# Kernel tuning notes

Hardware: AMD Instinct MI355X
Metric: run time of the kernel (lower is better)

Reference implementation:

```python
import jax, jax.numpy as jnp
import numpy as np

C = 3  # RGB channels

# Scharr kernels, depthwise: shape [C_out, C_in/groups, kh, kw] = [C, 1, 3, 3]
_KX = np.array([[-3., 0., 3.], [-10., 0., 10.], [-3., 0., 3.]], dtype=np.float32)
_KY = np.array([[-3., -10., -3.], [0., 0., 0.], [3., 10., 3.]], dtype=np.float32)
KERNEL_X = jnp.tile(jnp.asarray(_KX)[None, None], (C, 1, 1, 1))
KERNEL_Y = jnp.tile(jnp.asarray(_KY)[None, None], (C, 1, 1, 1))


def _depthwise3x3(img, kernel):
    # img: [B, C, H, W]; kernel: [C, 1, 3, 3]; groups=C, stride 1, padding 1
    return jax.lax.conv_general_dilated(
        img, kernel,
        window_strides=(1, 1),
        padding=((1, 1), (1, 1)),
        dimension_numbers=('NCHW', 'OIHW', 'NCHW'),
        feature_group_count=C)


def _scharr_grad(img):
    gx = _depthwise3x3(img, KERNEL_X)
    gy = _depthwise3x3(img, KERNEL_Y)
    return jnp.abs(gx) + jnp.abs(gy)


def setup_inputs() -> dict:
    key = jax.random.key(0)
    kx, kg = jax.random.split(key)
    x = jax.random.uniform(kx, (16, 3, 512, 512), dtype=jnp.float32)
    gt = jax.random.uniform(kg, (16, 3, 512, 512), dtype=jnp.float32)
    return {"x": x, "gt": gt}


def reference(x, gt):
    loss = jnp.abs(_scharr_grad(x) - _scharr_grad(gt))
    return jnp.mean(loss)  # size_average=True
```

## Files before the change

### kernel.cpp

```cpp
#include <hip/hip_runtime.h>

#define Wd 512
#define Hd 512
#define NIMG 48
#define RB 8
#define LR (RB + 2)
#define NBLK (NIMG * (Hd / RB))
constexpr float INV_N = 1.0f / (float)((long long)NIMG * Hd * Wd);

__device__ __forceinline__ void gload_lds16(const float* g, float* l) {
    __builtin_amdgcn_global_load_lds(
        (const __attribute__((address_space(1))) void*)g,
        (__attribute__((address_space(3))) void*)l, 16, 0, 0);
}

__device__ __forceinline__ float scharr_pix(const float r0[10], const float r1[10],
                                            const float r2[10], int j) {
    float tl = r0[j], tm = r0[j + 1], tr = r0[j + 2];
    float ml = r1[j],                  mr = r1[j + 2];
    float bl = r2[j], bm = r2[j + 1], br = r2[j + 2];
    float gx = 3.f * (tr - tl) + 10.f * (mr - ml) + 3.f * (br - bl);
    float gy = 3.f * (bl - tl) + 10.f * (bm - tm) + 3.f * (br - tr);
    return fabsf(gx) + fabsf(gy);
}

__device__ __forceinline__ void lds_row(const float* __restrict__ row, int lane,
                                        float r[10]) {
    float4 b0 = *reinterpret_cast<const float4*>(row + lane * 8);
    float4 b1 = *reinterpret_cast<const float4*>(row + lane * 8 + 4);
    r[1] = b0.x; r[2] = b0.y; r[3] = b0.z; r[4] = b0.w;
    r[5] = b1.x; r[6] = b1.y; r[7] = b1.z; r[8] = b1.w;
    float lv = __shfl_up(b1.w, 1, 64);
    float rv = __shfl_down(b0.x, 1, 64);
    r[0] = (lane > 0)  ? lv : 0.f;
    r[9] = (lane < 63) ? rv : 0.f;
}

__global__ void __launch_bounds__(256, 4)
scharr_loss_kernel(const float* __restrict__ x, const float* __restrict__ gt,
                   float* __restrict__ partials) {
    __shared__ float lb[2][LR][Wd];

    int wid  = threadIdx.x >> 6;
    int lane = threadIdx.x & 63;

    int b   = blockIdx.x;
    int swz = (b & 7) * (NBLK / 8) + (b >> 3);
    int img = swz >> 6;
    int h0  = (swz & 63) * RB;

    const float* __restrict__ xb = x  + (size_t)img * Hd * Wd;
    const float* __restrict__ gb = gt + (size_t)img * Hd * Wd;

    #pragma unroll
    for (int t = 0; t < 10; ++t) {
        int c    = wid + t * 4;
        int im   = (c >= 20) ? 1 : 0;
        int cc   = c - im * 20;
        int row  = cc >> 1;
        int half = cc & 1;
        int gh   = h0 - 1 + row;
        const float* __restrict__ sb = im ? gb : xb;
        float* dst = &lb[im][row][half * 256];
        if ((unsigned)gh < (unsigned)Hd) {
            gload_lds16(sb + (size_t)gh * Wd + half * 256 + lane * 4, dst);
        } else {
            *reinterpret_cast<float4*>(dst + lane * 4) =
                make_float4(0.f, 0.f, 0.f, 0.f);
        }
    }
    __syncthreads();

    int lr = wid * 2;
    float rx[3][10], rg[3][10];
    lds_row(&lb[0][lr][0],     lane, rx[0]);
    lds_row(&lb[0][lr + 1][0], lane, rx[1]);
    lds_row(&lb[1][lr][0],     lane, rg[0]);
    lds_row(&lb[1][lr + 1][0], lane, rg[1]);

    float sum = 0.f;
    #pragma unroll
    for (int i = 0; i < 2; ++i) {
        const int c0 = i % 3, c1 = (i + 1) % 3, c2 = (i + 2) % 3;
        lds_row(&lb[0][lr + i + 2][0], lane, rx[c2]);
        lds_row(&lb[1][lr + i + 2][0], lane, rg[c2]);
        #pragma unroll
        for (int j = 0; j < 8; ++j) {
            float a = scharr_pix(rx[c0], rx[c1], rx[c2], j);
            float g = scharr_pix(rg[c0], rg[c1], rg[c2], j);
            sum += fabsf(a - g);
        }
    }

    #pragma unroll
    for (int off = 32; off > 0; off >>= 1)
        sum += __shfl_down(sum, off, 64);
    __syncthreads();
    if (lane == 0) lb[0][0][wid] = sum;
    __syncthreads();
    if (threadIdx.x == 0)
        partials[blockIdx.x] = lb[0][0][0] + lb[0][0][1]
                             + lb[0][0][2] + lb[0][0][3];
}

__global__ void __launch_bounds__(256)
reduce_partials_kernel(const float* __restrict__ partials, float* __restrict__ out) {
    const float4* p4 = reinterpret_cast<const float4*>(partials);
    float s = 0.f;
    #pragma unroll
    for (int k = 0; k < NBLK / 4 / 256; ++k) {
        float4 v = p4[k * 256 + threadIdx.x];
        s += v.x + v.y + v.z + v.w;
    }
    #pragma unroll
    for (int off = 32; off > 0; off >>= 1)
        s += __shfl_down(s, off, 64);
    __shared__ float ws[4];
    int lane = threadIdx.x & 63;
    int wid  = threadIdx.x >> 6;
    if (lane == 0) ws[wid] = s;
    __syncthreads();
    if (threadIdx.x == 0)
        out[0] = (ws[0] + ws[1] + ws[2] + ws[3]) * INV_N;
}

extern "C" void kernel_launch(void* const* d_in, const int* in_sizes, int n_in,
                              void* d_out, int out_size, void* d_ws, size_t ws_size,
                              hipStream_t stream) {
    const float* x  = (const float*)d_in[0];
    const float* gt = (const float*)d_in[1];
    float* out      = (float*)d_out;
    float* partials = (float*)d_ws;

    scharr_loss_kernel<<<NBLK, 256, 0, stream>>>(x, gt, partials);
    reduce_partials_kernel<<<1, 256, 0, stream>>>(partials, out);
}
```

Baseline: 25.19 us.

## Double row tile to 16 rows with 512 threads and split-phase LDS loads

```diff
diff --git a/kernel.cpp b/kernel.cpp
--- a/kernel.cpp
+++ b/kernel.cpp
@@ -3,7 +3,7 @@
 #define Wd 512
 #define Hd 512
 #define NIMG 48
-#define RB 8
+#define RB 16
 #define LR (RB + 2)
 #define NBLK (NIMG * (Hd / RB))
 constexpr float INV_N = 1.0f / (float)((long long)NIMG * Hd * Wd);
@@ -36,25 +36,27 @@
     r[9] = (lane < 63) ? rv : 0.f;
 }
 
-__global__ void __launch_bounds__(256, 4)
+__global__ void __launch_bounds__(512, 4)
 scharr_loss_kernel(const float* __restrict__ x, const float* __restrict__ gt,
                    float* __restrict__ partials) {
     __shared__ float lb[2][LR][Wd];
+    __shared__ float ws[8];
 
     int wid  = threadIdx.x >> 6;
     int lane = threadIdx.x & 63;
 
-    int b   = blockIdx.x;
-    int swz = (b & 7) * (NBLK / 8) + (b >> 3);
-    int img = swz >> 6;
-    int h0  = (swz & 63) * RB;
+    int b    = blockIdx.x;
+    int swz  = (b & 7) * (NBLK / 8) + (b >> 3);
+    int img  = swz >> 5;
+    int trow = swz & 31;
+    int h0   = trow * RB;
 
     const float* __restrict__ xb = x  + (size_t)img * Hd * Wd;
     const float* __restrict__ gb = gt + (size_t)img * Hd * Wd;
 
     #pragma unroll
-    for (int t = 0; t < 10; ++t) {
-        int c    = wid + t * 4;
+    for (int t = 0; t < 5; ++t) {
+        int c    = wid + t * 8;
         int im   = (c >= 20) ? 1 : 0;
         int cc   = c - im * 20;
         int row  = cc >> 1;
@@ -69,49 +71,78 @@
                 make_float4(0.f, 0.f, 0.f, 0.f);
         }
     }
+    #pragma unroll
+    for (int t = 0; t < 4; ++t) {
+        int c    = wid + t * 8;
+        int im   = (c >= 16) ? 1 : 0;
+        int cc   = c - im * 16;
+        int row  = 10 + (cc >> 1);
+        int half = cc & 1;
+        int gh   = h0 - 1 + row;
+        const float* __restrict__ sb = im ? gb : xb;
+        float* dst = &lb[im][row][half * 256];
+        if ((unsigned)gh < (unsigned)Hd) {
+            gload_lds16(sb + (size_t)gh * Wd + half * 256 + lane * 4, dst);
+        } else {
+            *reinterpret_cast<float4*>(dst + lane * 4) =
+                make_float4(0.f, 0.f, 0.f, 0.f);
+        }
+    }
+
+    if (trow == 31) {
+        asm volatile("s_waitcnt vmcnt(2) lgkmcnt(0)" ::: "memory");
+    } else {
+        asm volatile("s_waitcnt vmcnt(4) lgkmcnt(0)" ::: "memory");
+    }
+    __builtin_amdgcn_sched_barrier(0);
+    __builtin_amdgcn_s_barrier();
+    __builtin_amdgcn_sched_barrier(0);
+
+    float sum = 0.f;
+    auto compute2 = [&](int lr) {
+        float rx[3][10], rg[3][10];
+        lds_row(&lb[0][lr][0],     lane, rx[0]);
+        lds_row(&lb[0][lr + 1][0], lane, rx[1]);
+        lds_row(&lb[1][lr][0],     lane, rg[0]);
+        lds_row(&lb[1][lr + 1][0], lane, rg[1]);
+        #pragma unroll
+        for (int i = 0; i < 2; ++i) {
+            const int c0 = i % 3, c1 = (i + 1) % 3, c2 = (i + 2) % 3;
+            lds_row(&lb[0][lr + i + 2][0], lane, rx[c2]);
+            lds_row(&lb[1][lr + i + 2][0], lane, rg[c2]);
+            #pragma unroll
+            for (int j = 0; j < 8; ++j) {
+                float a = scharr_pix(rx[c0], rx[c1], rx[c2], j);
+                float g = scharr_pix(rg[c0], rg[c1], rg[c2], j);
+                sum += fabsf(a - g);
+            }
+        }
+    };
+
+    if (wid < 4) compute2(wid * 2);
+
     __syncthreads();
 
-    int lr = wid * 2;
-    float rx[3][10], rg[3][10];
-    lds_row(&lb[0][lr][0],     lane, rx[0]);
-    lds_row(&lb[0][lr + 1][0], lane, rx[1]);
-    lds_row(&lb[1][lr][0],     lane, rg[0]);
-    lds_row(&lb[1][lr + 1][0], lane, rg[1]);
-
-    float sum = 0.f;
-    #pragma unroll
-    for (int i = 0; i < 2; ++i) {
-        const int c0 = i % 3, c1 = (i + 1) % 3, c2 = (i + 2) % 3;
-        lds_row(&lb[0][lr + i + 2][0], lane, rx[c2]);
-        lds_row(&lb[1][lr + i + 2][0], lane, rg[c2]);
-        #pragma unroll
-        for (int j = 0; j < 8; ++j) {
-            float a = scharr_pix(rx[c0], rx[c1], rx[c2], j);
-            float g = scharr_pix(rg[c0], rg[c1], rg[c2], j);
-            sum += fabsf(a - g);
-        }
-    }
+    if (wid >= 4) compute2(8 + (wid - 4) * 2);
 
     #pragma unroll
     for (int off = 32; off > 0; off >>= 1)
         sum += __shfl_down(sum, off, 64);
+    if (lane == 0) ws[wid] = sum;
     __syncthreads();
-    if (lane == 0) lb[0][0][wid] = sum;
-    __syncthreads();
-    if (threadIdx.x == 0)
-        partials[blockIdx.x] = lb[0][0][0] + lb[0][0][1]
-                             + lb[0][0][2] + lb[0][0][3];
+    if (threadIdx.x == 0) {
+        float s = ws[0] + ws[1] + ws[2] + ws[3]
+                + ws[4] + ws[5] + ws[6] + ws[7];
+        partials[blockIdx.x] = s;
+    }
 }
 
 __global__ void __launch_bounds__(256)
 reduce_partials_kernel(const float* __restrict__ partials, float* __restrict__ out) {
-    const float4* p4 = reinterpret_cast<const float4*>(partials);
     float s = 0.f;
     #pragma unroll
-    for (int k = 0; k < NBLK / 4 / 256; ++k) {
-        float4 v = p4[k * 256 + threadIdx.x];
-        s += v.x + v.y + v.z + v.w;
-    }
+    for (int k = 0; k < NBLK / 256; ++k)
+        s += partials[k * 256 + threadIdx.x];
     #pragma unroll
     for (int off = 32; off > 0; off >>= 1)
         s += __shfl_down(s, off, 64);
@@ -132,6 +163,6 @@
     float* out      = (float*)d_out;
     float* partials = (float*)d_ws;
 
-    scharr_loss_kernel<<<NBLK, 256, 0, stream>>>(x, gt, partials);
+    scharr_loss_kernel<<<NBLK, 512, 0, stream>>>(x, gt, partials);
     reduce_partials_kernel<<<1, 256, 0, stream>>>(partials, out);
 }
```

Result: slower. 27.71 us (+10.0%).
